# Optimization experiments

Measured on AMD Instinct MI355X. Metric: run time of the kernel, lower is better.

## Reference

```python
import jax, jax.numpy as jnp
import numpy as np

B, NX, NC, C, H = 4, 1024, 2048, 1024, 16
DH = C // H            # head_dim = 64
SCALE = DH ** -0.5


def setup_inputs() -> dict:
    key = jax.random.key(0)
    ks = jax.random.split(key, 6)
    # sorted unique token indices to update per batch (== positions where update_mask==1)
    rng = np.random.default_rng(0)
    idx = np.stack([np.sort(rng.permutation(NC)[:NX]) for _ in range(B)]).astype(np.int32)
    return {
        "x": jax.random.normal(ks[0], (B, NX, C), jnp.float32),
        "update_idx": jnp.asarray(idx),                              # (B, NX) int32
        "cache_k": jax.random.normal(ks[1], (B, H, NC, DH), jnp.float32),
        "cache_v": jax.random.normal(ks[2], (B, H, NC, DH), jnp.float32),
        "w_qkv": jax.random.normal(ks[3], (3 * C, C), jnp.float32) * 0.02,
        "b_qkv": jnp.zeros((3 * C,), jnp.float32),
        "w_proj": jax.random.normal(ks[4], (C, C), jnp.float32) * 0.02,
        "b_proj": jnp.zeros((C,), jnp.float32),
    }


def reference(x, update_idx, cache_k, cache_v, w_qkv, b_qkv, w_proj, b_proj):
    Bq, N, Cq = x.shape
    # QKV projection: (B, N, 3C) -> (3, B, H, N, Dh) layout as in torch permute(2,0,3,1,4)
    qkv = (x @ w_qkv.T + b_qkv).reshape(Bq, N, 3, H, DH)
    q = qkv[:, :, 0].transpose(0, 2, 1, 3)  # (B, H, N, Dh)
    k = qkv[:, :, 1].transpose(0, 2, 1, 3)
    v = qkv[:, :, 2].transpose(0, 2, 1, 3)
    # masked_scatter_ of k/v into cache at the masked (updated) token slots.
    # Indices are sorted, so row-order masked_scatter == indexed scatter.
    scat = jax.vmap(lambda cache, idx, src: cache.at[:, idx, :].set(src))
    k_full = scat(cache_k, update_idx, k)    # (B, H, NC, Dh)
    v_full = scat(cache_v, update_idx, v)
    # plain attention: q scaled, full softmax over cache length
    attn = jax.nn.softmax(jnp.einsum('bhqd,bhkd->bhqk', q * SCALE, k_full), axis=-1)
    out = jnp.einsum('bhqk,bhkd->bhqd', attn, v_full)  # (B, H, N, Dh)
    out = out.transpose(0, 2, 1, 3).reshape(Bq, N, Cq)
    return out @ w_proj.T + b_proj
```

## Files before the change

kernel.cpp:

```cpp
#include <hip/hip_runtime.h>
#include <hip/hip_bf16.h>

#define B_   4
#define NX_  1024
#define NC_  2048
#define C_   1024
#define H_   16
#define DH_  64

typedef __attribute__((ext_vector_type(8))) __bf16 bf16x8;
typedef __attribute__((ext_vector_type(4))) float  f32x4;

static __device__ __forceinline__ unsigned short f2bf(float f) {
    unsigned int u = __float_as_uint(f);
    u += 0x7fffu + ((u >> 16) & 1u);
    return (unsigned short)(u >> 16);
}

static __device__ __forceinline__ unsigned int pk2(float lo, float hi) {
    unsigned int a = __float_as_uint(lo) + 0x8000u;
    unsigned int b = __float_as_uint(hi) + 0x8000u;
    return __builtin_amdgcn_perm(b, a, 0x07060302);
}

static __device__ __forceinline__ unsigned int cvtpk(float lo, float hi) {
    unsigned int r;
    asm("v_cvt_pk_bf16_f32 %0, %1, %2" : "=v"(r) : "v"(lo), "v"(hi));
    return r;
}

static __device__ __forceinline__ bf16x8 ldfrag(const unsigned short* p) {
    union { uint4 u; bf16x8 b; } cv;
    cv.u = *reinterpret_cast<const uint4*>(p);
    return cv.b;
}

__global__ __launch_bounds__(256) void cvt_all_kernel(
    const float* __restrict__ x,  const float* __restrict__ wq,
    const float* __restrict__ wp, const float* __restrict__ ck,
    const float* __restrict__ cv_,
    unsigned short* __restrict__ xbf,  unsigned short* __restrict__ wqbf,
    unsigned short* __restrict__ wpbf, unsigned short* __restrict__ kfb,
    unsigned short* __restrict__ vt) {
    int blk = blockIdx.x;
    if (blk < 16384) {
        const float* src; unsigned short* dst; int i;
        if (blk < 4096)      { src = x;  dst = xbf;  i = blk; }
        else if (blk < 7168) { src = wq; dst = wqbf; i = blk - 4096; }
        else if (blk < 8192) { src = wp; dst = wpbf; i = blk - 7168; }
        else                 { src = ck; dst = kfb;  i = blk - 8192; }
        int idx = i * 256 + threadIdx.x;
        float4 f = reinterpret_cast<const float4*>(src)[idx];
        ushort4 o;
        o.x = f2bf(f.x); o.y = f2bf(f.y); o.z = f2bf(f.z); o.w = f2bf(f.w);
        reinterpret_cast<ushort4*>(dst)[idx] = o;
    } else {
        int i   = blk - 16384;
        int t   = threadIdx.x;
        int bh  = i >> 6;
        int kg  = i & 63;
        int d   = t & 63;
        int kci = t >> 6;
        int kc  = kg * 4 + kci;
        const float* src = cv_ + ((size_t)bh * NC_ + (size_t)kc * 8) * DH_ + d;
        union { uint4 u; unsigned short s[8]; } o;
#pragma unroll
        for (int j = 0; j < 8; j++) o.s[j] = f2bf(src[(size_t)j * DH_]);
        *reinterpret_cast<uint4*>(vt + ((size_t)bh * DH_ + d) * NC_ + (size_t)kc * 8) = o.u;
    }
}

#define LSTR 40

__global__ __launch_bounds__(256, 3) void qkv_gemm_kernel(
    const unsigned short* __restrict__ xbf,
    const unsigned short* __restrict__ wbf,
    const float* __restrict__ bias,
    const int* __restrict__ uidx,
    unsigned short* __restrict__ qb,
    unsigned short* __restrict__ kf,
    unsigned short* __restrict__ vt)
{
    __shared__ unsigned short As[128 * LSTR], Bs[128 * LSTR];
    __shared__ int jtab[128];
    int bn = blockIdx.x, bm = blockIdx.y;
    int w = threadIdx.x >> 6, l = threadIdx.x & 63;
    int quad = l >> 4, col = l & 15;
    int wr = w >> 1, wc = w & 1;
    int srow = w * 32 + (l >> 2), schk = (l & 3) * 8;

    const unsigned short* Ap = xbf + (size_t)(bm * 128 + srow) * C_ + schk;
    const unsigned short* Bp = wbf + (size_t)(bn * 128 + srow) * C_ + schk;
    unsigned short* Aw = As + srow * LSTR + schk;
    unsigned short* Bw = Bs + srow * LSTR + schk;

    f32x4 acc[4][4];
#pragma unroll
    for (int a = 0; a < 4; a++)
#pragma unroll
        for (int b = 0; b < 4; b++) acc[a][b] = (f32x4){0.f, 0.f, 0.f, 0.f};

    uint4 ar0, ar1, br0, br1;
#define LDREG(kk_)                                                       \
    {   int kk = (kk_) * 32;                                             \
        ar0 = *reinterpret_cast<const uint4*>(Ap + kk);                  \
        ar1 = *reinterpret_cast<const uint4*>(Ap + 16 * C_ + kk);        \
        br0 = *reinterpret_cast<const uint4*>(Bp + kk);                  \
        br1 = *reinterpret_cast<const uint4*>(Bp + 16 * C_ + kk);        \
    }
#define WRTILE()                                                         \
    {   *reinterpret_cast<uint4*>(Aw)             = ar0;                 \
        *reinterpret_cast<uint4*>(Aw + 16 * LSTR) = ar1;                 \
        *reinterpret_cast<uint4*>(Bw)             = br0;                 \
        *reinterpret_cast<uint4*>(Bw + 16 * LSTR) = br1;                 \
    }

    LDREG(0);
    WRTILE();
    LDREG(1);
    __syncthreads();
#pragma unroll 1
    for (int it = 0; it < 32; it++) {
        bf16x8 af[4], bfr[4];
#pragma unroll
        for (int t = 0; t < 4; t++) af[t]  = ldfrag(&As[(wr * 64 + t * 16 + col) * LSTR + quad * 8]);
#pragma unroll
        for (int t = 0; t < 4; t++) bfr[t] = ldfrag(&Bs[(wc * 64 + t * 16 + col) * LSTR + quad * 8]);
#pragma unroll
        for (int mt = 0; mt < 4; mt++)
#pragma unroll
            for (int nt = 0; nt < 4; nt++)
                acc[mt][nt] = __builtin_amdgcn_mfma_f32_16x16x32_bf16(af[mt], bfr[nt], acc[mt][nt], 0, 0, 0);
        if (it < 31) {
            __syncthreads();
            WRTILE();
            LDREG(it + 2 < 31 ? it + 2 : 31);
            __syncthreads();
        }
    }
#undef LDREG
#undef WRTILE

    int part = bn >> 3;
    float bv[4];
#pragma unroll
    for (int nt = 0; nt < 4; nt++) bv[nt] = bias[bn * 128 + wc * 64 + nt * 16 + col];

    if (part <= 1) {
        int nl[4];
#pragma unroll
        for (int nt = 0; nt < 4; nt++) nl[nt] = (bn * 128 + wc * 64 + nt * 16 + col) & 1023;
        const float QS = 0.18033688011112042f;
#pragma unroll
        for (int mt = 0; mt < 4; mt++)
#pragma unroll
            for (int r = 0; r < 4; r++) {
                int m = bm * 128 + wr * 64 + mt * 16 + quad * 4 + r;
                int b = m >> 10, i = m & 1023;
                int j = (part == 0) ? 0 : uidx[m];
#pragma unroll
                for (int nt = 0; nt < 4; nt++) {
                    int h = nl[nt] >> 6, d = nl[nt] & 63;
                    float v = acc[mt][nt][r] + bv[nt];
                    if (part == 0)
                        qb[((size_t)(b * H_ + h) * NX_ + i) * DH_ + d] = f2bf(v * QS);
                    else
                        kf[((size_t)(b * H_ + h) * NC_ + j) * DH_ + d] = f2bf(v);
                }
            }
    } else {
        if (threadIdx.x < 128) jtab[threadIdx.x] = uidx[bm * 128 + threadIdx.x];
        __syncthreads();
        int h = ((bn * 128 + wc * 64) & 1023) >> 6;
        int b = (bm * 128) >> 10;
        unsigned short* T = (wc == 0) ? As : Bs;
        int jv = jtab[wr * 64 + l];
        unsigned short* vb2 = vt + ((size_t)(b * H_ + h) * 64) * NC_ + jv;
#pragma unroll 1
        for (int round = 0; round < 2; round++) {
            if (wr == round) {
#pragma unroll
                for (int nt = 0; nt < 4; nt++)
#pragma unroll
                    for (int mt = 0; mt < 4; mt++) {
                        uint2 pk;
                        pk.x = pk2(acc[mt][nt][0] + bv[nt], acc[mt][nt][1] + bv[nt]);
                        pk.y = pk2(acc[mt][nt][2] + bv[nt], acc[mt][nt][3] + bv[nt]);
                        *reinterpret_cast<uint2*>(&T[(nt * 16 + col) * 72 + mt * 16 + quad * 4]) = pk;
                    }
                asm volatile("s_waitcnt lgkmcnt(0)" ::: "memory");
#pragma unroll 1
                for (int d = 0; d < 64; d++)
                    vb2[(size_t)d * NC_] = T[d * 72 + l];
            }
            __syncthreads();
        }
    }
}

__global__ __launch_bounds__(256, 4) void attn_kernel(
    const unsigned short* __restrict__ qb,
    const unsigned short* __restrict__ kf,
    const unsigned short* __restrict__ vt,
    unsigned short* __restrict__ ao)
{
    __shared__ __align__(16) char smem[20480];
    unsigned short* Klo = (unsigned short*)smem;
    unsigned short* Khi = Klo + 64 * LSTR;
    unsigned short* V0s = Khi + 64 * LSTR;
    unsigned short* V1s = V0s + 64 * LSTR;
    float* Om = (float*)smem;
    float* Lm = Om + 2 * 32 * 64;

    int id = blockIdx.x;
    int qt = (id >> 3) & 15;
    int bh = ((id >> 7) << 3) | (id & 7);
    int wave = threadIdx.x >> 6, lane = threadIdx.x & 63;
    int quad = lane >> 4, col = lane & 15;
    int qh = wave & 1;
    int kh = wave >> 1;
    int srow = wave * 16 + (lane >> 2), schk = (lane & 3) * 8;
    int L = lane & 3;
    int ve0 = (L < 2) ? 16 * L : 16 * L - 28;
    int ve1 = ve0 + 8;

    const unsigned short* qrow0 = qb + ((size_t)bh * NX_ + qt * 64 + qh * 32 + col) * DH_;
    bf16x8 qfA[2], qfB[2];
    qfA[0] = ldfrag(qrow0 + quad * 8);
    qfB[0] = ldfrag(qrow0 + 32 + quad * 8);
    qfA[1] = ldfrag(qrow0 + 16 * DH_ + quad * 8);
    qfB[1] = ldfrag(qrow0 + 16 * DH_ + 32 + quad * 8);

    const unsigned short* Kp = kf + ((size_t)bh * NC_ + srow) * DH_ + schk;
    const unsigned short* Vp = vt + ((size_t)bh * DH_ + srow) * NC_ + schk;
    unsigned short* Kwl = Klo + srow * LSTR + schk;
    unsigned short* Kwh = Khi + srow * LSTR + schk;
    unsigned short* Vw0 = V0s + srow * LSTR;
    unsigned short* Vw1 = V1s + srow * LSTR;
    const unsigned short* Vs = kh ? V1s : V0s;
    int kq = kh * 32;

    f32x4 o[4][2];
#pragma unroll
    for (int m = 0; m < 4; m++)
#pragma unroll
        for (int n = 0; n < 2; n++) o[m][n] = (f32x4){0.f, 0.f, 0.f, 0.f};
    f32x4 lacc[2];
    lacc[0] = (f32x4){0.f, 0.f, 0.f, 0.f};
    lacc[1] = (f32x4){0.f, 0.f, 0.f, 0.f};
    bf16x8 onef;
    { union { unsigned int u[4]; bf16x8 b; } c1;
      c1.u[0] = c1.u[1] = c1.u[2] = c1.u[3] = 0x3F803F80u; onef = c1.b; }

    uint4 kr0, kr1, vr0, vr1;
#define LDREG(kb_)                                                        \
    {   kr0 = *reinterpret_cast<const uint4*>(Kp + (size_t)(kb_) * 64 * DH_);      \
        kr1 = *reinterpret_cast<const uint4*>(Kp + (size_t)(kb_) * 64 * DH_ + 32); \
        vr0 = *reinterpret_cast<const uint4*>(Vp + (kb_) * 64);           \
        vr1 = *reinterpret_cast<const uint4*>(Vp + (kb_) * 64 + 32);      \
    }
#define WRTILE()                                                          \
    {   *reinterpret_cast<uint4*>(Kwl) = kr0;                             \
        *reinterpret_cast<uint4*>(Kwh) = kr1;                             \
        uint2 t_;                                                         \
        t_.x = vr0.x; t_.y = vr0.y; *reinterpret_cast<uint2*>(Vw0 + ve0) = t_; \
        t_.x = vr0.z; t_.y = vr0.w; *reinterpret_cast<uint2*>(Vw0 + ve1) = t_; \
        t_.x = vr1.x; t_.y = vr1.y; *reinterpret_cast<uint2*>(Vw1 + ve0) = t_; \
        t_.x = vr1.z; t_.y = vr1.w; *reinterpret_cast<uint2*>(Vw1 + ve1) = t_; \
    }

    LDREG(0);
    WRTILE();
    LDREG(1);
    __syncthreads();

#pragma unroll 1
    for (int kb = 0; kb < 32; kb++) {
        f32x4 s[2][2];
#pragma unroll
        for (int mt = 0; mt < 2; mt++)
#pragma unroll
            for (int nt = 0; nt < 2; nt++) s[mt][nt] = (f32x4){0.f, 0.f, 0.f, 0.f};
#pragma unroll
        for (int mt = 0; mt < 2; mt++) {
            bf16x8 ka = ldfrag(&Klo[(kq + mt * 16 + col) * LSTR + quad * 8]);
            bf16x8 kb_ = ldfrag(&Khi[(kq + mt * 16 + col) * LSTR + quad * 8]);
#pragma unroll
            for (int nt = 0; nt < 2; nt++) {
                s[mt][nt] = __builtin_amdgcn_mfma_f32_16x16x32_bf16(ka,  qfA[nt], s[mt][nt], 0, 0, 0);
                s[mt][nt] = __builtin_amdgcn_mfma_f32_16x16x32_bf16(kb_, qfB[nt], s[mt][nt], 0, 0, 0);
            }
        }
        bf16x8 vfr[4];
#pragma unroll
        for (int t = 0; t < 4; t++) vfr[t] = ldfrag(&Vs[(t * 16 + col) * LSTR + quad * 8]);
        bf16x8 pf[2];
#pragma unroll
        for (int nt = 0; nt < 2; nt++) {
            float e0 = exp2f(s[0][nt][0]), e1 = exp2f(s[0][nt][1]);
            float e2 = exp2f(s[0][nt][2]), e3 = exp2f(s[0][nt][3]);
            float e4 = exp2f(s[1][nt][0]), e5 = exp2f(s[1][nt][1]);
            float e6 = exp2f(s[1][nt][2]), e7 = exp2f(s[1][nt][3]);
            union { unsigned int u[4]; bf16x8 b; } pw;
            pw.u[0] = cvtpk(e0, e1);
            pw.u[1] = cvtpk(e2, e3);
            pw.u[2] = cvtpk(e4, e5);
            pw.u[3] = cvtpk(e6, e7);
            pf[nt] = pw.b;
        }
        lacc[0] = __builtin_amdgcn_mfma_f32_16x16x32_bf16(onef, pf[0], lacc[0], 0, 0, 0);
        lacc[1] = __builtin_amdgcn_mfma_f32_16x16x32_bf16(onef, pf[1], lacc[1], 0, 0, 0);
#pragma unroll
        for (int mt = 0; mt < 4; mt++) {
            o[mt][0] = __builtin_amdgcn_mfma_f32_16x16x32_bf16(vfr[mt], pf[0], o[mt][0], 0, 0, 0);
            o[mt][1] = __builtin_amdgcn_mfma_f32_16x16x32_bf16(vfr[mt], pf[1], o[mt][1], 0, 0, 0);
        }
        if (kb < 31) {
            __syncthreads();
            WRTILE();
            LDREG(kb + 2 < 31 ? kb + 2 : 31);
            __syncthreads();
        }
    }
#undef LDREG
#undef WRTILE

    float l_i[2] = { lacc[0][0], lacc[1][0] };

    __syncthreads();
    if (kh == 1) {
#pragma unroll
        for (int mt = 0; mt < 4; mt++)
#pragma unroll
            for (int nt = 0; nt < 2; nt++)
#pragma unroll
                for (int r = 0; r < 4; r++)
                    Om[(qh * 32 + (mt * 2 + nt) * 4 + r) * 64 + lane] = o[mt][nt][r];
        if (quad == 0) {
            Lm[(qh * 2 + 0) * 16 + col] = l_i[0];
            Lm[(qh * 2 + 1) * 16 + col] = l_i[1];
        }
    }
    __syncthreads();
    if (kh == 0) {
        float inv[2];
#pragma unroll
        for (int nt = 0; nt < 2; nt++)
            inv[nt] = 1.f / (l_i[nt] + Lm[(qh * 2 + nt) * 16 + col]);
        int b = bh >> 4, h = bh & 15;
#pragma unroll
        for (int mt = 0; mt < 4; mt++)
#pragma unroll
            for (int nt = 0; nt < 2; nt++) {
                int base = (qh * 32 + (mt * 2 + nt) * 4) * 64 + lane;
                float v0 = (o[mt][nt][0] + Om[base])       * inv[nt];
                float v1 = (o[mt][nt][1] + Om[base + 64])  * inv[nt];
                float v2 = (o[mt][nt][2] + Om[base + 128]) * inv[nt];
                float v3 = (o[mt][nt][3] + Om[base + 192]) * inv[nt];
                int q = qt * 64 + qh * 32 + nt * 16 + col;
                uint2 ov;
                ov.x = pk2(v0, v1);
                ov.y = pk2(v2, v3);
                *reinterpret_cast<uint2*>(ao + ((size_t)b * NX_ + q) * C_ +
                                          h * 64 + mt * 16 + quad * 4) = ov;
            }
    }
}

__global__ __launch_bounds__(256, 3) void proj_gemm_kernel(
    const unsigned short* __restrict__ abf,
    const unsigned short* __restrict__ wbf,
    const float* __restrict__ bias,
    float* __restrict__ out)
{
    __shared__ unsigned short As[128 * LSTR], Bs[64 * LSTR];
    int bn = blockIdx.x, bm = blockIdx.y;
    int w = threadIdx.x >> 6, l = threadIdx.x & 63;
    int quad = l >> 4, col = l & 15;
    int sarow = w * 32 + (l >> 2), sbrow = w * 16 + (l >> 2), schk = (l & 3) * 8;

    const unsigned short* Ap = abf + (size_t)(bm * 128 + sarow) * C_ + schk;
    const unsigned short* Bp = wbf + (size_t)(bn * 64 + sbrow) * C_ + schk;
    unsigned short* Aw = As + sarow * LSTR + schk;
    unsigned short* Bw = Bs + sbrow * LSTR + schk;

    f32x4 acc[2][4];
#pragma unroll
    for (int a = 0; a < 2; a++)
#pragma unroll
        for (int b = 0; b < 4; b++) acc[a][b] = (f32x4){0.f, 0.f, 0.f, 0.f};

    uint4 ar0, ar1, br0;
#define LDREG(kk_)                                                       \
    {   int kk = (kk_) * 32;                                             \
        ar0 = *reinterpret_cast<const uint4*>(Ap + kk);                  \
        ar1 = *reinterpret_cast<const uint4*>(Ap + 16 * C_ + kk);        \
        br0 = *reinterpret_cast<const uint4*>(Bp + kk);                  \
    }
#define WRTILE()                                                         \
    {   *reinterpret_cast<uint4*>(Aw)             = ar0;                 \
        *reinterpret_cast<uint4*>(Aw + 16 * LSTR) = ar1;                 \
        *reinterpret_cast<uint4*>(Bw)             = br0;                 \
    }

    LDREG(0);
    WRTILE();
    LDREG(1);
    __syncthreads();
#pragma unroll 1
    for (int it = 0; it < 32; it++) {
        bf16x8 af[2], bfr[4];
#pragma unroll
        for (int t = 0; t < 2; t++) af[t]  = ldfrag(&As[(w * 32 + t * 16 + col) * LSTR + quad * 8]);
#pragma unroll
        for (int t = 0; t < 4; t++) bfr[t] = ldfrag(&Bs[(t * 16 + col) * LSTR + quad * 8]);
#pragma unroll
        for (int mt = 0; mt < 2; mt++)
#pragma unroll
            for (int nt = 0; nt < 4; nt++)
                acc[mt][nt] = __builtin_amdgcn_mfma_f32_16x16x32_bf16(af[mt], bfr[nt], acc[mt][nt], 0, 0, 0);
        if (it < 31) {
            __syncthreads();
            WRTILE();
            LDREG(it + 2 < 31 ? it + 2 : 31);
            __syncthreads();
        }
    }
#undef LDREG
#undef WRTILE

    float bv[4];
#pragma unroll
    for (int nt = 0; nt < 4; nt++) bv[nt] = bias[bn * 64 + nt * 16 + col];
#pragma unroll
    for (int mt = 0; mt < 2; mt++)
#pragma unroll
        for (int r = 0; r < 4; r++) {
            int m = bm * 128 + w * 32 + mt * 16 + quad * 4 + r;
#pragma unroll
            for (int nt = 0; nt < 4; nt++) {
                int n = bn * 64 + nt * 16 + col;
                out[(size_t)m * C_ + n] = acc[mt][nt][r] + bv[nt];
            }
        }
}

extern "C" void kernel_launch(void* const* d_in, const int* in_sizes, int n_in,
                              void* d_out, int out_size, void* d_ws, size_t ws_size,
                              hipStream_t stream) {
    const float* x      = (const float*)d_in[0];
    const int*   uidx   = (const int*)  d_in[1];
    const float* cachek = (const float*)d_in[2];
    const float* cachev = (const float*)d_in[3];
    const float* wqkv   = (const float*)d_in[4];
    const float* bqkv   = (const float*)d_in[5];
    const float* wproj  = (const float*)d_in[6];
    const float* bproj  = (const float*)d_in[7];
    float* out = (float*)d_out;

    char* ws = (char*)d_ws;
    unsigned short* xbf  = (unsigned short*)(ws);
    unsigned short* wqbf = (unsigned short*)(ws + (8ull  << 20));
    unsigned short* wpbf = (unsigned short*)(ws + (14ull << 20));
    unsigned short* qb   = (unsigned short*)(ws + (16ull << 20));
    unsigned short* kfb  = (unsigned short*)(ws + (24ull << 20));
    unsigned short* vtb  = (unsigned short*)(ws + (40ull << 20));
    unsigned short* aob  = (unsigned short*)(ws + (56ull << 20));

    cvt_all_kernel<<<20480, 256, 0, stream>>>(x, wqkv, wproj, cachek, cachev,
                                              xbf, wqbf, wpbf, kfb, vtb);
    qkv_gemm_kernel <<<dim3(24, 32), 256, 0, stream>>>(xbf, wqbf, bqkv, uidx, qb, kfb, vtb);
    attn_kernel     <<<1024, 256, 0, stream>>>(qb, kfb, vtb, aob);
    proj_gemm_kernel<<<dim3(16, 32), 256, 0, stream>>>(aob, wpbf, bproj, out);
}
```

Before: 250.9 us.

## Use direct global-to-LDS loads with double buffering in QKV and proj GEMMs

Result: no change. 255.1 us (+1.7%).

```diff
diff --git a/kernel.cpp b/kernel.cpp
--- a/kernel.cpp
+++ b/kernel.cpp
@@ -33,6 +33,12 @@
     union { uint4 u; bf16x8 b; } cv;
     cv.u = *reinterpret_cast<const uint4*>(p);
     return cv.b;
+}
+
+#define AS1 __attribute__((address_space(1)))
+#define AS3 __attribute__((address_space(3)))
+static __device__ __forceinline__ void gload16(const unsigned short* g, unsigned short* l) {
+    __builtin_amdgcn_global_load_lds((const AS1 void*)g, (AS3 void*)l, 16, 0, 0);
 }
 
 __global__ __launch_bounds__(256) void cvt_all_kernel(
@@ -81,18 +87,16 @@
     unsigned short* __restrict__ kf,
     unsigned short* __restrict__ vt)
 {
-    __shared__ unsigned short As[128 * LSTR], Bs[128 * LSTR];
+    __shared__ unsigned short SA[2][128 * 32], SB[2][128 * 32];
     __shared__ int jtab[128];
     int bn = blockIdx.x, bm = blockIdx.y;
     int w = threadIdx.x >> 6, l = threadIdx.x & 63;
     int quad = l >> 4, col = l & 15;
     int wr = w >> 1, wc = w & 1;
-    int srow = w * 32 + (l >> 2), schk = (l & 3) * 8;
+    int srow = w * 16 + (l >> 2), schk = (l & 3) * 8;
 
     const unsigned short* Ap = xbf + (size_t)(bm * 128 + srow) * C_ + schk;
     const unsigned short* Bp = wbf + (size_t)(bn * 128 + srow) * C_ + schk;
-    unsigned short* Aw = As + srow * LSTR + schk;
-    unsigned short* Bw = Bs + srow * LSTR + schk;
 
     f32x4 acc[4][4];
 #pragma unroll
@@ -100,46 +104,35 @@
 #pragma unroll
         for (int b = 0; b < 4; b++) acc[a][b] = (f32x4){0.f, 0.f, 0.f, 0.f};
 
-    uint4 ar0, ar1, br0, br1;
-#define LDREG(kk_)                                                       \
-    {   int kk = (kk_) * 32;                                             \
-        ar0 = *reinterpret_cast<const uint4*>(Ap + kk);                  \
-        ar1 = *reinterpret_cast<const uint4*>(Ap + 16 * C_ + kk);        \
-        br0 = *reinterpret_cast<const uint4*>(Bp + kk);                  \
-        br1 = *reinterpret_cast<const uint4*>(Bp + 16 * C_ + kk);        \
-    }
-#define WRTILE()                                                         \
-    {   *reinterpret_cast<uint4*>(Aw)             = ar0;                 \
-        *reinterpret_cast<uint4*>(Aw + 16 * LSTR) = ar1;                 \
-        *reinterpret_cast<uint4*>(Bw)             = br0;                 \
-        *reinterpret_cast<uint4*>(Bw + 16 * LSTR) = br1;                 \
-    }
-
-    LDREG(0);
-    WRTILE();
-    LDREG(1);
+    auto stage = [&](int p, int kk) {
+        const unsigned short* a0 = Ap + kk * 32;
+        const unsigned short* b0 = Bp + kk * 32;
+        unsigned short* da = &SA[p][w * 512];
+        unsigned short* db = &SB[p][w * 512];
+        gload16(a0,            da);
+        gload16(a0 + 64 * C_,  da + 2048);
+        gload16(b0,            db);
+        gload16(b0 + 64 * C_,  db + 2048);
+    };
+
+    stage(0, 0);
     __syncthreads();
 #pragma unroll 1
     for (int it = 0; it < 32; it++) {
+        if (it < 31) stage((it + 1) & 1, it + 1);
+        int p = it & 1;
         bf16x8 af[4], bfr[4];
 #pragma unroll
-        for (int t = 0; t < 4; t++) af[t]  = ldfrag(&As[(wr * 64 + t * 16 + col) * LSTR + quad * 8]);
-#pragma unroll
-        for (int t = 0; t < 4; t++) bfr[t] = ldfrag(&Bs[(wc * 64 + t * 16 + col) * LSTR + quad * 8]);
+        for (int t = 0; t < 4; t++) af[t]  = ldfrag(&SA[p][(wr * 64 + t * 16 + col) * 32 + quad * 8]);
+#pragma unroll
+        for (int t = 0; t < 4; t++) bfr[t] = ldfrag(&SB[p][(wc * 64 + t * 16 + col) * 32 + quad * 8]);
 #pragma unroll
         for (int mt = 0; mt < 4; mt++)
 #pragma unroll
             for (int nt = 0; nt < 4; nt++)
                 acc[mt][nt] = __builtin_amdgcn_mfma_f32_16x16x32_bf16(af[mt], bfr[nt], acc[mt][nt], 0, 0, 0);
-        if (it < 31) {
-            __syncthreads();
-            WRTILE();
-            LDREG(it + 2 < 31 ? it + 2 : 31);
-            __syncthreads();
-        }
-    }
-#undef LDREG
-#undef WRTILE
+        __syncthreads();
+    }
 
     int part = bn >> 3;
     float bv[4];
@@ -173,7 +166,7 @@
         __syncthreads();
         int h = ((bn * 128 + wc * 64) & 1023) >> 6;
         int b = (bm * 128) >> 10;
-        unsigned short* T = (wc == 0) ? As : Bs;
+        unsigned short* T = (wc == 0) ? &SA[0][0] : &SB[0][0];
         int jv = jtab[wr * 64 + l];
         unsigned short* vb2 = vt + ((size_t)(b * H_ + h) * 64) * NC_ + jv;
 #pragma unroll 1
@@ -373,16 +366,14 @@
     const float* __restrict__ bias,
     float* __restrict__ out)
 {
-    __shared__ unsigned short As[128 * LSTR], Bs[64 * LSTR];
+    __shared__ unsigned short SA[2][128 * 32], SB[2][64 * 32];
     int bn = blockIdx.x, bm = blockIdx.y;
     int w = threadIdx.x >> 6, l = threadIdx.x & 63;
     int quad = l >> 4, col = l & 15;
-    int sarow = w * 32 + (l >> 2), sbrow = w * 16 + (l >> 2), schk = (l & 3) * 8;
-
-    const unsigned short* Ap = abf + (size_t)(bm * 128 + sarow) * C_ + schk;
-    const unsigned short* Bp = wbf + (size_t)(bn * 64 + sbrow) * C_ + schk;
-    unsigned short* Aw = As + sarow * LSTR + schk;
-    unsigned short* Bw = Bs + sbrow * LSTR + schk;
+    int srow = w * 16 + (l >> 2), schk = (l & 3) * 8;
+
+    const unsigned short* Ap = abf + (size_t)(bm * 128 + srow) * C_ + schk;
+    const unsigned short* Bp = wbf + (size_t)(bn * 64 + srow) * C_ + schk;
 
     f32x4 acc[2][4];
 #pragma unroll
@@ -390,44 +381,33 @@
 #pragma unroll
         for (int b = 0; b < 4; b++) acc[a][b] = (f32x4){0.f, 0.f, 0.f, 0.f};
 
-    uint4 ar0, ar1, br0;
-#define LDREG(kk_)                                                       \
-    {   int kk = (kk_) * 32;                                             \
-        ar0 = *reinterpret_cast<const uint4*>(Ap + kk);                  \
-        ar1 = *reinterpret_cast<const uint4*>(Ap + 16 * C_ + kk);        \
-        br0 = *reinterpret_cast<const uint4*>(Bp + kk);                  \
-    }
-#define WRTILE()                                                         \
-    {   *reinterpret_cast<uint4*>(Aw)             = ar0;                 \
-        *reinterpret_cast<uint4*>(Aw + 16 * LSTR) = ar1;                 \
-        *reinterpret_cast<uint4*>(Bw)             = br0;                 \
-    }
-
-    LDREG(0);
-    WRTILE();
-    LDREG(1);
+    auto stage = [&](int p, int kk) {
+        const unsigned short* a0 = Ap + kk * 32;
+        const unsigned short* b0 = Bp + kk * 32;
+        unsigned short* da = &SA[p][w * 512];
+        gload16(a0,           da);
+        gload16(a0 + 64 * C_, da + 2048);
+        gload16(b0,           &SB[p][w * 512]);
+    };
+
+    stage(0, 0);
     __syncthreads();
 #pragma unroll 1
     for (int it = 0; it < 32; it++) {
+        if (it < 31) stage((it + 1) & 1, it + 1);
+        int p = it & 1;
         bf16x8 af[2], bfr[4];
 #pragma unroll
-        for (int t = 0; t < 2; t++) af[t]  = ldfrag(&As[(w * 32 + t * 16 + col) * LSTR + quad * 8]);
-#pragma unroll
-        for (int t = 0; t < 4; t++) bfr[t] = ldfrag(&Bs[(t * 16 + col) * LSTR + quad * 8]);
+        for (int t = 0; t < 2; t++) af[t]  = ldfrag(&SA[p][(w * 32 + t * 16 + col) * 32 + quad * 8]);
+#pragma unroll
+        for (int t = 0; t < 4; t++) bfr[t] = ldfrag(&SB[p][(t * 16 + col) * 32 + quad * 8]);
 #pragma unroll
         for (int mt = 0; mt < 2; mt++)
 #pragma unroll
             for (int nt = 0; nt < 4; nt++)
                 acc[mt][nt] = __builtin_amdgcn_mfma_f32_16x16x32_bf16(af[mt], bfr[nt], acc[mt][nt], 0, 0, 0);
-        if (it < 31) {
-            __syncthreads();
-            WRTILE();
-            LDREG(it + 2 < 31 ? it + 2 : 31);
-            __syncthreads();
-        }
-    }
-#undef LDREG
-#undef WRTILE
+        __syncthreads();
+    }
 
     float bv[4];
 #pragma unroll
```

## Split attention key range across two wave groups per block with shared-memory reduction

Applied to the files above, without the earlier changes.

Result: slower. 655.5 us (+161.3%).

```diff
diff --git a/kernel.cpp b/kernel.cpp
--- a/kernel.cpp
+++ b/kernel.cpp
@@ -198,17 +198,13 @@
     }
 }
 
-__global__ __launch_bounds__(256, 4) void attn_kernel(
+__global__ __launch_bounds__(512, 8) void attn_kernel(
     const unsigned short* __restrict__ qb,
     const unsigned short* __restrict__ kf,
     const unsigned short* __restrict__ vt,
     unsigned short* __restrict__ ao)
 {
-    __shared__ __align__(16) char smem[20480];
-    unsigned short* Klo = (unsigned short*)smem;
-    unsigned short* Khi = Klo + 64 * LSTR;
-    unsigned short* V0s = Khi + 64 * LSTR;
-    unsigned short* V1s = V0s + 64 * LSTR;
+    __shared__ __align__(16) char smem[2 * 20480];
     float* Om = (float*)smem;
     float* Lm = Om + 2 * 32 * 64;
 
@@ -218,11 +214,18 @@
     int wave = threadIdx.x >> 6, lane = threadIdx.x & 63;
     int quad = lane >> 4, col = lane & 15;
     int qh = wave & 1;
-    int kh = wave >> 1;
-    int srow = wave * 16 + (lane >> 2), schk = (lane & 3) * 8;
+    int kh = (wave >> 1) & 1;
+    int ks = wave >> 2;
+    int srow = (wave & 3) * 16 + (lane >> 2), schk = (lane & 3) * 8;
     int L = lane & 3;
     int ve0 = (L < 2) ? 16 * L : 16 * L - 28;
     int ve1 = ve0 + 8;
+
+    unsigned short* G = (unsigned short*)smem + ks * 10240;
+    unsigned short* Klo = G;
+    unsigned short* Khi = G + 64 * LSTR;
+    unsigned short* V0s = G + 2 * 64 * LSTR;
+    unsigned short* V1s = G + 3 * 64 * LSTR;
 
     const unsigned short* qrow0 = qb + ((size_t)bh * NX_ + qt * 64 + qh * 32 + col) * DH_;
     bf16x8 qfA[2], qfB[2];
@@ -231,8 +234,8 @@
     qfA[1] = ldfrag(qrow0 + 16 * DH_ + quad * 8);
     qfB[1] = ldfrag(qrow0 + 16 * DH_ + 32 + quad * 8);
 
-    const unsigned short* Kp = kf + ((size_t)bh * NC_ + srow) * DH_ + schk;
-    const unsigned short* Vp = vt + ((size_t)bh * DH_ + srow) * NC_ + schk;
+    const unsigned short* Kp = kf + ((size_t)bh * NC_ + ks * 1024 + srow) * DH_ + schk;
+    const unsigned short* Vp = vt + ((size_t)bh * DH_ + srow) * NC_ + ks * 1024 + schk;
     unsigned short* Kwl = Klo + srow * LSTR + schk;
     unsigned short* Kwh = Khi + srow * LSTR + schk;
     unsigned short* Vw0 = V0s + srow * LSTR;
@@ -253,11 +256,11 @@
       c1.u[0] = c1.u[1] = c1.u[2] = c1.u[3] = 0x3F803F80u; onef = c1.b; }
 
     uint4 kr0, kr1, vr0, vr1;
-#define LDREG(kb_)                                                        \
-    {   kr0 = *reinterpret_cast<const uint4*>(Kp + (size_t)(kb_) * 64 * DH_);      \
-        kr1 = *reinterpret_cast<const uint4*>(Kp + (size_t)(kb_) * 64 * DH_ + 32); \
-        vr0 = *reinterpret_cast<const uint4*>(Vp + (kb_) * 64);           \
-        vr1 = *reinterpret_cast<const uint4*>(Vp + (kb_) * 64 + 32);      \
+#define LDREG(t_)                                                         \
+    {   kr0 = *reinterpret_cast<const uint4*>(Kp + (size_t)(t_) * 64 * DH_);      \
+        kr1 = *reinterpret_cast<const uint4*>(Kp + (size_t)(t_) * 64 * DH_ + 32); \
+        vr0 = *reinterpret_cast<const uint4*>(Vp + (t_) * 64);            \
+        vr1 = *reinterpret_cast<const uint4*>(Vp + (t_) * 64 + 32);       \
     }
 #define WRTILE()                                                          \
     {   *reinterpret_cast<uint4*>(Kwl) = kr0;                             \
@@ -275,7 +278,7 @@
     __syncthreads();
 
 #pragma unroll 1
-    for (int kb = 0; kb < 32; kb++) {
+    for (int t = 0; t < 16; t++) {
         f32x4 s[2][2];
 #pragma unroll
         for (int mt = 0; mt < 2; mt++)
@@ -283,7 +286,7 @@
             for (int nt = 0; nt < 2; nt++) s[mt][nt] = (f32x4){0.f, 0.f, 0.f, 0.f};
 #pragma unroll
         for (int mt = 0; mt < 2; mt++) {
-            bf16x8 ka = ldfrag(&Klo[(kq + mt * 16 + col) * LSTR + quad * 8]);
+            bf16x8 ka  = ldfrag(&Klo[(kq + mt * 16 + col) * LSTR + quad * 8]);
             bf16x8 kb_ = ldfrag(&Khi[(kq + mt * 16 + col) * LSTR + quad * 8]);
 #pragma unroll
             for (int nt = 0; nt < 2; nt++) {
@@ -293,7 +296,7 @@
         }
         bf16x8 vfr[4];
 #pragma unroll
-        for (int t = 0; t < 4; t++) vfr[t] = ldfrag(&Vs[(t * 16 + col) * LSTR + quad * 8]);
+        for (int tt = 0; tt < 4; tt++) vfr[tt] = ldfrag(&Vs[(tt * 16 + col) * LSTR + quad * 8]);
         bf16x8 pf[2];
 #pragma unroll
         for (int nt = 0; nt < 2; nt++) {
@@ -315,10 +318,10 @@
             o[mt][0] = __builtin_amdgcn_mfma_f32_16x16x32_bf16(vfr[mt], pf[0], o[mt][0], 0, 0, 0);
             o[mt][1] = __builtin_amdgcn_mfma_f32_16x16x32_bf16(vfr[mt], pf[1], o[mt][1], 0, 0, 0);
         }
-        if (kb < 31) {
+        if (t < 15) {
             __syncthreads();
             WRTILE();
-            LDREG(kb + 2 < 31 ? kb + 2 : 31);
+            LDREG(t + 2 < 15 ? t + 2 : 15);
             __syncthreads();
         }
     }
@@ -328,7 +331,7 @@
     float l_i[2] = { lacc[0][0], lacc[1][0] };
 
     __syncthreads();
-    if (kh == 1) {
+    if (ks == 1 && kh == 1) {
 #pragma unroll
         for (int mt = 0; mt < 4; mt++)
 #pragma unroll
@@ -342,7 +345,35 @@
         }
     }
     __syncthreads();
-    if (kh == 0) {
+    if (ks == 0 && kh == 1) {
+#pragma unroll
+        for (int mt = 0; mt < 4; mt++)
+#pragma unroll
+            for (int nt = 0; nt < 2; nt++)
+#pragma unroll
+                for (int r = 0; r < 4; r++)
+                    Om[(qh * 32 + (mt * 2 + nt) * 4 + r) * 64 + lane] += o[mt][nt][r];
+        if (quad == 0) {
+            Lm[(qh * 2 + 0) * 16 + col] += l_i[0];
+            Lm[(qh * 2 + 1) * 16 + col] += l_i[1];
+        }
+    }
+    __syncthreads();
+    if (ks == 1 && kh == 0) {
+#pragma unroll
+        for (int mt = 0; mt < 4; mt++)
+#pragma unroll
+            for (int nt = 0; nt < 2; nt++)
+#pragma unroll
+                for (int r = 0; r < 4; r++)
+                    Om[(qh * 32 + (mt * 2 + nt) * 4 + r) * 64 + lane] += o[mt][nt][r];
+        if (quad == 0) {
+            Lm[(qh * 2 + 0) * 16 + col] += l_i[0];
+            Lm[(qh * 2 + 1) * 16 + col] += l_i[1];
+        }
+    }
+    __syncthreads();
+    if (ks == 0 && kh == 0) {
         float inv[2];
 #pragma unroll
         for (int nt = 0; nt < 2; nt++)
@@ -470,6 +501,6 @@
     cvt_all_kernel<<<20480, 256, 0, stream>>>(x, wqkv, wproj, cachek, cachev,
                                               xbf, wqbf, wpbf, kfb, vtb);
     qkv_gemm_kernel <<<dim3(24, 32), 256, 0, stream>>>(xbf, wqbf, bqkv, uidx, qb, kfb, vtb);
-    attn_kernel     <<<1024, 256, 0, stream>>>(qb, kfb, vtb, aob);
+    attn_kernel     <<<1024, 512, 0, stream>>>(qb, kfb, vtb, aob);
     proj_gemm_kernel<<<dim3(16, 32), 256, 0, stream>>>(aob, wpbf, bproj, out);
 }
```
